# Performance work log

Measured on AMD Instinct MI355X. Metric: run time of the kernel, lower is better.

The kernel has to match this reference:

```python
import jax, jax.numpy as jnp
import numpy as np

B, V, T = 8, 25, 128
C, NH, DK = 256, 8, 32      # hidden_size = NH*DK; dv == dk (required by residual shapes)
DFF, IT = 1024, 4           # FFN hidden (d_in), num_layers
EPS_LN, EPS_BN, SLOPE = 1e-6, 1e-5, 0.01
SCALE = np.float32(1.0 / np.sqrt(DK))


def setup_inputs():
    ks = iter(jax.random.split(jax.random.key(0), 40))
    def w(shape, s=0.05):
        return jax.random.normal(next(ks), shape, jnp.float32) * s
    inp = {'data': jax.random.normal(next(ks), (B, C, V, T), jnp.float32)}
    inp['ln_g'] = jnp.ones((IT, C)); inp['ln_b'] = jnp.zeros((IT, C))
    for p in ('tj', 'tr'):
        for nm in ('q', 'k', 'v'):
            inp[p + '_w' + nm] = w((IT, C, C))
            inp[p + '_b' + nm] = jnp.zeros((IT, C))
        inp[p + '_bn_g'] = jnp.ones((IT, C)); inp[p + '_bn_b'] = jnp.zeros((IT, C))
        inp[p + '_w1'] = w((IT, DFF, C)); inp[p + '_b1'] = jnp.zeros((IT, DFF))
        inp[p + '_w2'] = w((IT, C, DFF)); inp[p + '_b2'] = jnp.zeros((IT, C))
        inp[p + '_fbn_g'] = jnp.ones((IT, C)); inp[p + '_fbn_b'] = jnp.zeros((IT, C))
    return inp


def _bn(x, g, b, axes):
    # train-mode BatchNorm: batch stats, biased variance; channel axis = 1
    m = x.mean(axes, keepdims=True)
    v = ((x - m) ** 2).mean(axes, keepdims=True)
    sh = [1] * x.ndim; sh[1] = -1
    return (x - m) * jax.lax.rsqrt(v + EPS_BN) * g.reshape(sh) + b.reshape(sh)


def _ffn(x, w1, b1, w2, b2, fg, fb):
    # PositionFeedForward on x: [N, C, L] -> [N, C, L]
    xt = jnp.swapaxes(x, 1, 2)                                   # [N, L, C]
    h = jax.nn.relu(jnp.einsum('nlc,fc->nlf', xt, w1) + b1)
    o = jnp.einsum('nlf,cf->nlc', h, w2) + b2 + xt               # residual
    return _bn(jnp.swapaxes(o, 1, 2), fg, fb, (0, 2))


def _tju(x, ax, wq, bq, wk, bk, wv, bv, bn_g, bn_b, w1, b1, w2, b2, fg, fb):
    # sliding-window (3) self-attn + 2 relay tokens; x: [N,C,T], ax: [N,C,2,T]
    N = x.shape[0]
    q = (jnp.einsum('oc,nct->not', wq, x) + bq[:, None]).reshape(N, NH, DK, T)
    k = (jnp.einsum('oc,nct->not', wk, x) + bk[:, None]).reshape(N, NH, DK, T)
    v = (jnp.einsum('oc,nct->not', wv, x) + bv[:, None]).reshape(N, NH, DK, T)
    kp = jnp.pad(k, ((0, 0), (0, 0), (0, 0), (1, 1)))
    vp = jnp.pad(v, ((0, 0), (0, 0), (0, 0), (1, 1)))
    kw = jnp.stack([kp[..., u:u + T] for u in range(3)], axis=3)  # [N,NH,DK,3,T]
    vw = jnp.stack([vp[..., u:u + T] for u in range(3)], axis=3)
    ak = (jnp.einsum('oc,ncat->noat', wk, ax) + bk[:, None, None]).reshape(N, NH, DK, 2, T)
    av = (jnp.einsum('oc,ncat->noat', wv, ax) + bv[:, None, None]).reshape(N, NH, DK, 2, T)
    kk = jnp.concatenate([kw, ak], axis=3)                        # [N,NH,DK,5,T]
    vv = jnp.concatenate([vw, av], axis=3)
    a = jax.nn.softmax(jnp.einsum('nhdt,nhdwt->nhwt', q, kk) * SCALE, axis=2)
    att = jnp.einsum('nhwt,nhdwt->nhdt', a, vv).reshape(N, C, T)
    ret = _bn(x + att, bn_g, bn_b, (0, 2))
    return _ffn(ret, w1, b1, w2, b2, fg, fb)


def _tru(r, y, wq, bq, wk, bk, wv, bv, bn_g, bn_b, w1, b1, w2, b2, fg, fb):
    # relay cross-attention; r: [N,C], y: [N,C,L]
    N, _, L = y.shape
    q = (r @ wq.T + bq).reshape(N, NH, DK)
    k = (jnp.einsum('oc,ncl->nol', wk, y) + bk[:, None]).reshape(N, NH, DK, L)
    v = (jnp.einsum('oc,ncl->nol', wv, y) + bv[:, None]).reshape(N, NH, DK, L)
    a = jax.nn.softmax(jnp.einsum('nhd,nhdl->nhl', q, k) * SCALE, axis=-1)
    att = jnp.einsum('nhl,nhdl->nhd', a, v).reshape(N, C)
    ret = _bn((r + att)[:, :, None], bn_g, bn_b, (0, 2))          # BN over batch
    return _ffn(ret, w1, b1, w2, b2, fg, fb)[:, :, 0]


def _forward(data, ln_g, ln_b, tj, tr):
    N = B * V
    embs = jnp.transpose(data, (0, 2, 1, 3)).reshape(N, C, T)
    nodes, relay = embs, embs.mean(2)                             # relay: [N,C]
    for i in range(IT):
        ax = jnp.concatenate([embs[:, :, None, :],
                              jnp.broadcast_to(relay[:, :, None, None], (N, C, 1, T))], axis=2)
        m = nodes.mean(1, keepdims=True)
        vv = nodes.var(1, keepdims=True)
        xln = (nodes - m) * jax.lax.rsqrt(vv + EPS_LN) * ln_g[i][None, :, None] + ln_b[i][None, :, None]
        nodes = jax.nn.leaky_relu(_tju(xln, ax, *[p[i] for p in tj]), SLOPE)
        y = jnp.concatenate([relay[:, :, None], nodes], axis=2)   # [N,C,T+1]
        relay = jax.nn.leaky_relu(_tru(relay, y, *[p[i] for p in tr]), SLOPE)
    return nodes.reshape(B, V, C, T)


def reference(data, ln_g, ln_b,
              tj_wq, tj_bq, tj_wk, tj_bk, tj_wv, tj_bv, tj_bn_g, tj_bn_b,
              tj_w1, tj_b1, tj_w2, tj_b2, tj_fbn_g, tj_fbn_b,
              tr_wq, tr_bq, tr_wk, tr_bk, tr_wv, tr_bv, tr_bn_g, tr_bn_b,
              tr_w1, tr_b1, tr_w2, tr_b2, tr_fbn_g, tr_fbn_b):
    tj = (tj_wq, tj_bq, tj_wk, tj_bk, tj_wv, tj_bv, tj_bn_g, tj_bn_b,
          tj_w1, tj_b1, tj_w2, tj_b2, tj_fbn_g, tj_fbn_b)
    tr = (tr_wq, tr_bq, tr_wk, tr_bk, tr_wv, tr_bv, tr_bn_g, tr_bn_b,
          tr_w1, tr_b1, tr_w2, tr_b2, tr_fbn_g, tr_fbn_b)
    return _forward(data, ln_g, ln_b, tj, tr)
```

## Files before the change

kernel.cpp:

```cpp
#include <hip/hip_runtime.h>
#include <cstddef>

#define BB   8
#define VV   25
#define TT   128
#define CC   256
#define NHH  8
#define DKK  32
#define DFFF 1024
#define ITER 4
#define NN   (BB*VV)
#define NT   (NN*TT)
#define LL1  (TT+1)
#define EPS_LN 1e-6f
#define EPS_BN 1e-5f
#define SLOPE  0.01f
#define SCALE_F 0.17677669529663687f

typedef unsigned short ushort_t;
typedef __attribute__((ext_vector_type(8))) short short8;
typedef __attribute__((ext_vector_type(4))) short short4_t;
typedef __attribute__((ext_vector_type(4))) float floatx4;

union U8 { short8 v; ushort_t u[8]; };

__device__ __forceinline__ float bf2f(ushort_t u) {
    union { unsigned int i; float f; } x; x.i = ((unsigned int)u) << 16; return x.f;
}
__device__ __forceinline__ ushort_t f2bf(float f) {
    union { float f; unsigned int i; } x; x.f = f;
    unsigned int r = x.i + 0x7FFFu + ((x.i >> 16) & 1u);
    return (ushort_t)(r >> 16);
}
__device__ __forceinline__ float2 bn_fin(float s, float ss) {
    float m = s * (1.0f/NT);
    float var = ss * (1.0f/NT) - m*m; if (var < 0.f) var = 0.f;
    return make_float2(m, rsqrtf(var + EPS_BN));
}

__device__ __forceinline__ void gl_lds16(const ushort_t* g, ushort_t* l) {
    __builtin_amdgcn_global_load_lds(
        (const __attribute__((address_space(1))) unsigned int*)g,
        (__attribute__((address_space(3))) unsigned int*)l,
        16, 0, 0);
}

__device__ __forceinline__ void ld32(const ushort_t* p, float* q) {
    #pragma unroll
    for (int c8 = 0; c8 < 4; c8++) {
        U8 u; u.v = *(const short8*)(p + c8*8);
        #pragma unroll
        for (int j = 0; j < 8; j++) q[c8*8+j] = bf2f(u.u[j]);
    }
}
__device__ __forceinline__ float dot32(const ushort_t* p, const float* q) {
    float s = 0.f;
    #pragma unroll
    for (int c8 = 0; c8 < 4; c8++) {
        U8 u; u.v = *(const short8*)(p + c8*8);
        #pragma unroll
        for (int j = 0; j < 8; j++) s += q[c8*8+j]*bf2f(u.u[j]);
    }
    return s;
}
__device__ __forceinline__ void acc32(const ushort_t* p, float e, float* av) {
    #pragma unroll
    for (int c8 = 0; c8 < 4; c8++) {
        U8 u; u.v = *(const short8*)(p + c8*8);
        #pragma unroll
        for (int j = 0; j < 8; j++) av[c8*8+j] += e*bf2f(u.u[j]);
    }
}

__global__ __launch_bounds__(256) void k_zero(float* __restrict__ p, int n)
{
    int i = blockIdx.x*256 + threadIdx.x;
    if (i < n) p[i] = 0.f;
}
__global__ __launch_bounds__(256) void k_cast2(const float* __restrict__ src,
    ushort_t* __restrict__ dst, int per, int dstride, int total)
{
    int i = blockIdx.x*256 + threadIdx.x;
    if (i < total) dst[(size_t)(i/per)*dstride + (i%per)] = f2bf(src[i]);
}
__global__ __launch_bounds__(256) void k_copy2(const float* __restrict__ src,
    float* __restrict__ dst, int per, int dstride, int total)
{
    int i = blockIdx.x*256 + threadIdx.x;
    if (i < total) dst[(size_t)(i/per)*dstride + (i%per)] = src[i];
}

__global__ __launch_bounds__(128) void k_embed(const float* __restrict__ data,
    float* __restrict__ nodesf, ushort_t* __restrict__ embs_bf, float* __restrict__ relay)
{
    __shared__ float tile[32][TT+1];
    int cc0 = blockIdx.x*32, n = blockIdx.y;
    int b = n / VV, v = n % VV, t = threadIdx.x;
    for (int cl = 0; cl < 32; cl++)
        tile[cl][t] = data[(((size_t)b*CC + cc0 + cl)*VV + v)*TT + t];
    __syncthreads();
    if (t < 32) {
        float s = 0.f;
        for (int tt = 0; tt < TT; tt++) s += tile[t][tt];
        relay[n*CC + cc0 + t] = s * (1.0f/TT);
    }
    #pragma unroll 8
    for (int it = 0; it < 32; it++) {
        int t_l = it*4 + (t >> 5), c_l = t & 31;
        float val = tile[c_l][t_l];
        size_t o = (size_t)(n*TT + t_l)*CC + cc0 + c_l;
        nodesf[o] = val;
        embs_bf[o] = f2bf(val);
    }
}

__global__ __launch_bounds__(256) void k_layernorm(float* __restrict__ x,
    ushort_t* __restrict__ outb, const float* __restrict__ g, const float* __restrict__ b)
{
    int wave = threadIdx.x >> 6, lane = threadIdx.x & 63;
    size_t base = (size_t)(blockIdx.x*4 + wave)*CC + lane*4;
    float4 v = *(float4*)&x[base];
    float s  = v.x + v.y + v.z + v.w;
    float ss = v.x*v.x + v.y*v.y + v.z*v.z + v.w*v.w;
    #pragma unroll
    for (int o = 32; o; o >>= 1) { s += __shfl_xor(s, o); ss += __shfl_xor(ss, o); }
    float m = s * (1.0f/CC);
    float var = ss * (1.0f/CC) - m*m; if (var < 0.f) var = 0.f;
    float rs = rsqrtf(var + EPS_LN);
    float4 gg = *(const float4*)&g[lane*4];
    float4 bb = *(const float4*)&b[lane*4];
    v.x = (v.x - m)*rs*gg.x + bb.x;
    v.y = (v.y - m)*rs*gg.y + bb.y;
    v.z = (v.z - m)*rs*gg.z + bb.z;
    v.w = (v.w - m)*rs*gg.w + bb.w;
    *(float4*)&x[base] = v;
    ushort_t o4[4] = {f2bf(v.x), f2bf(v.y), f2bf(v.z), f2bf(v.w)};
    *(short4_t*)&outb[base] = *(short4_t*)o4;
}

#define FL_RELU  1
#define FL_BF16  2
#define FL_RESBN 4
#define FL_HM    8

#define STAGE(SA, SB, T_) do {                                              \
    gl_lds16(aSrc[0] + (T_)*32, &SA[dstOff[0]]);                            \
    gl_lds16(bSrc[0] + (T_)*32, &SB[dstOff[0]]);                            \
    gl_lds16(aSrc[1] + (T_)*32, &SA[dstOff[1]]);                            \
    gl_lds16(bSrc[1] + (T_)*32, &SB[dstOff[1]]);                            \
    } while (0)

#define COMPUTE(SA, SB) do {                                                \
    short8 af_[4], bf_[4];                                                  \
    _Pragma("unroll")                                                       \
    for (int mi_ = 0; mi_ < 4; mi_++)                                       \
        af_[mi_] = *(const short8*)&SA[aOff[mi_]];                          \
    _Pragma("unroll")                                                       \
    for (int ni_ = 0; ni_ < 4; ni_++)                                       \
        bf_[ni_] = *(const short8*)&SB[bOff[ni_]];                          \
    _Pragma("unroll")                                                       \
    for (int mi_ = 0; mi_ < 4; mi_++)                                       \
        _Pragma("unroll")                                                   \
        for (int ni_ = 0; ni_ < 4; ni_++)                                   \
            acc[mi_][ni_] = __builtin_amdgcn_mfma_f32_16x16x32_bf16(        \
                bf_[ni_], af_[mi_], acc[mi_][ni_], 0, 0, 0);                \
    } while (0)

#define PHASE(CA, CB, PA, PB, T_) do {                                      \
    if ((T_) + 2 < NK) STAGE(PA, PB, (T_) + 2);                             \
    COMPUTE(CA, CB);                                                        \
    if ((T_) + 1 < NK) {                                                    \
        __builtin_amdgcn_sched_barrier(0);                                  \
        if ((T_) + 2 < NK)                                                  \
            asm volatile("s_waitcnt vmcnt(4) lgkmcnt(0)" ::: "memory");     \
        else                                                                \
            asm volatile("s_waitcnt vmcnt(0) lgkmcnt(0)" ::: "memory");     \
        __builtin_amdgcn_s_barrier();                                       \
        __builtin_amdgcn_sched_barrier(0);                                  \
    }                                                                       \
    } while (0)

template<int K, int STATS>
__global__ __launch_bounds__(256) void k_gemm_mfma(
    const ushort_t* A, const ushort_t* B, const float* bias,
    const float* rx, const float* __restrict__ rawms,
    const float* __restrict__ bng, const float* __restrict__ bnb,
    float* outf, ushort_t* outb, int ostride, int ntiles_n, int flags,
    const ushort_t* A2, const ushort_t* B2, const float* bias2,
    ushort_t* outb2, int ostride2, int ntiles_n2,
    float* stats_acc)
{
    __shared__ ushort_t sA0[128*32];
    __shared__ ushort_t sB0[128*32];
    __shared__ ushort_t sA1[128*32];
    __shared__ ushort_t sB1[128*32];
    __shared__ ushort_t sA2[128*32];
    __shared__ ushort_t sB2[128*32];
    const int pid = blockIdx.x;
    const int xcd = pid & 7, idx = pid >> 3;
    const int ntile_tot = ntiles_n + ntiles_n2;
    const int nt_i = idx % ntile_tot;
    const int m0 = (xcd*25 + idx/ntile_tot) * 128;
    const ushort_t* Ap;  const ushort_t* Bp;  const float* biasp;
    ushort_t* outbp;  int ostridep, n0;
    if (nt_i < ntiles_n) {
        Ap = A;  Bp = B;  biasp = bias;  outbp = outb;
        ostridep = ostride;  n0 = nt_i*128;
    } else {
        Ap = A2; Bp = B2; biasp = bias2; outbp = outb2;
        ostridep = ostride2; n0 = (nt_i - ntiles_n)*128;
    }
    const int tid = threadIdx.x;
    const int lane = tid & 63, wave = tid >> 6;
    const int wm = (wave & 1) * 64, wn = (wave >> 1) * 64;
    const int fr = lane >> 4, fc = lane & 15;

    const ushort_t* aSrc[2];
    const ushort_t* bSrc[2];
    int dstOff[2];
    #pragma unroll
    for (int j = 0; j < 2; j++) {
        int s = wave*128 + j*64 + lane;
        int row = s >> 2;
        int kcs = ((s & 3) - (row >> 1)) & 3;
        aSrc[j] = Ap + (size_t)(m0 + row)*K + kcs*8;
        bSrc[j] = Bp + (size_t)(n0 + row)*K + kcs*8;
        dstOff[j] = (wave*128 + j*64)*8;
    }
    int aOff[4], bOff[4];
    #pragma unroll
    for (int mi = 0; mi < 4; mi++) {
        int row = wm + mi*16 + fc;
        aOff[mi] = row*32 + (((fr + (row >> 1)) & 3) * 8);
    }
    #pragma unroll
    for (int ni = 0; ni < 4; ni++) {
        int row = wn + ni*16 + fc;
        bOff[ni] = row*32 + (((fr + (row >> 1)) & 3) * 8);
    }

    floatx4 acc[4][4];
    #pragma unroll
    for (int i = 0; i < 4; i++)
        #pragma unroll
        for (int j = 0; j < 4; j++) acc[i][j] = (floatx4){0.f,0.f,0.f,0.f};

    constexpr int NK = K >> 5;
    STAGE(sA0, sB0, 0);
    if (NK > 1) STAGE(sA1, sB1, 1);
    __builtin_amdgcn_sched_barrier(0);
    if (NK > 1) asm volatile("s_waitcnt vmcnt(4)" ::: "memory");
    else        asm volatile("s_waitcnt vmcnt(0)" ::: "memory");
    __builtin_amdgcn_s_barrier();
    __builtin_amdgcn_sched_barrier(0);

    #pragma unroll
    for (int tb = 0; tb < NK; tb += 3) {
        PHASE(sA0, sB0, sA2, sB2, tb);
        if (tb + 1 < NK) PHASE(sA1, sB1, sA0, sB0, tb + 1);
        if (tb + 2 < NK) PHASE(sA2, sB2, sA1, sB1, tb + 2);
    }

    float st[4][4], sst[4][4];
    if constexpr (STATS) {
        #pragma unroll
        for (int a = 0; a < 4; a++)
            #pragma unroll
            for (int b2_ = 0; b2_ < 4; b2_++) { st[a][b2_] = 0.f; sst[a][b2_] = 0.f; }
    }
    #pragma unroll
    for (int ni = 0; ni < 4; ni++) {
        int nb = n0 + wn + ni*16 + fr*4;
        float4 bias4 = *(const float4*)&biasp[nb];
        float bm[4] = {0,0,0,0}, bs[4] = {0,0,0,0}, bb2[4] = {0,0,0,0};
        if (flags & FL_RESBN) {
            float4 s1 = *(const float4*)&rawms[nb];
            float4 s2 = *(const float4*)&rawms[CC + nb];
            float4 g4 = *(const float4*)&bng[nb];
            float4 b4 = *(const float4*)&bnb[nb];
            float2 f0 = bn_fin(s1.x, s2.x); float2 f1 = bn_fin(s1.y, s2.y);
            float2 f2 = bn_fin(s1.z, s2.z); float2 f3 = bn_fin(s1.w, s2.w);
            bm[0]=f0.x; bm[1]=f1.x; bm[2]=f2.x; bm[3]=f3.x;
            bs[0]=f0.y*g4.x; bs[1]=f1.y*g4.y; bs[2]=f2.y*g4.z; bs[3]=f3.y*g4.w;
            bb2[0]=b4.x; bb2[1]=b4.y; bb2[2]=b4.z; bb2[3]=b4.w;
        }
        float bia[4] = {bias4.x, bias4.y, bias4.z, bias4.w};
        size_t hm_base = ((size_t)(nb >> 5) * NT) * 32 + (nb & 31);
        #pragma unroll
        for (int mi = 0; mi < 4; mi++) {
            int m = m0 + wm + mi*16 + fc;
            size_t idx2 = (flags & FL_HM) ? hm_base + (size_t)m*32
                                          : (size_t)m*ostridep + nb;
            float vals[4];
            #pragma unroll
            for (int r = 0; r < 4; r++) vals[r] = acc[mi][ni][r] + bia[r];
            if (flags & FL_RESBN) {
                float4 rx4 = *(const float4*)&rx[idx2];
                float rxa[4] = {rx4.x, rx4.y, rx4.z, rx4.w};
                #pragma unroll
                for (int r = 0; r < 4; r++)
                    vals[r] += (rxa[r] - bm[r])*bs[r] + bb2[r];
            }
            if (flags & FL_RELU)
                #pragma unroll
                for (int r = 0; r < 4; r++) vals[r] = fmaxf(vals[r], 0.f);
            if constexpr (STATS) {
                #pragma unroll
                for (int r = 0; r < 4; r++) {
                    st[ni][r] += vals[r];
                    sst[ni][r] += vals[r]*vals[r];
                }
            }
            if (flags & FL_BF16) {
                ushort_t o4[4] = {f2bf(vals[0]), f2bf(vals[1]),
                                  f2bf(vals[2]), f2bf(vals[3])};
                *(short4_t*)&outbp[idx2] = *(short4_t*)o4;
            } else {
                float4 ov = make_float4(vals[0], vals[1], vals[2], vals[3]);
                *(float4*)&outf[idx2] = ov;
            }
        }
    }
    if constexpr (STATS) {
        #pragma unroll
        for (int ni = 0; ni < 4; ni++)
            #pragma unroll
            for (int r = 0; r < 4; r++) {
                float s_ = st[ni][r], ss_ = sst[ni][r];
                #pragma unroll
                for (int msk = 1; msk < 16; msk <<= 1) {
                    s_  += __shfl_xor(s_,  msk);
                    ss_ += __shfl_xor(ss_, msk);
                }
                st[ni][r] = s_; sst[ni][r] = ss_;
            }
        if (fc == 0) {
            #pragma unroll
            for (int ni = 0; ni < 4; ni++)
                #pragma unroll
                for (int r = 0; r < 4; r++) {
                    int ch = n0 + wn + ni*16 + fr*4 + r;
                    atomicAdd(&stats_acc[ch],      st[ni][r]);
                    atomicAdd(&stats_acc[CC + ch], sst[ni][r]);
                }
        }
    }
}

__global__ __launch_bounds__(256) void k_sgemm(
    const float* __restrict__ W, const float* __restrict__ X,
    const float* __restrict__ bias, const float* __restrict__ res,
    float* __restrict__ out, int K, int OUT, int do_relu)
{
    __shared__ float sW[16][260];
    __shared__ float sX[16][260];
    int o0 = blockIdx.x*16, n0 = blockIdx.y*16;
    int tx = threadIdx.x, ty = threadIdx.y;
    int tid = ty*16 + tx;
    float acc0 = 0.f, acc1 = 0.f;
    for (int kc = 0; kc < K; kc += 256) {
        #pragma unroll
        for (int j = 0; j < 4; j++) {
            int lin = tid + j*256;
            int row = lin >> 6, c4 = (lin & 63)*4;
            *(float4*)&sW[row][c4] = *(const float4*)&W[(size_t)(o0+row)*K + kc + c4];
            float4 xv = make_float4(0.f,0.f,0.f,0.f);
            if (n0 + row < NN) xv = *(const float4*)&X[(size_t)(n0+row)*K + kc + c4];
            *(float4*)&sX[row][c4] = xv;
        }
        __syncthreads();
        #pragma unroll 8
        for (int k4 = 0; k4 < 64; k4 += 2) {
            float4 w0 = *(const float4*)&sW[tx][k4*4];
            float4 x0 = *(const float4*)&sX[ty][k4*4];
            float4 w1 = *(const float4*)&sW[tx][k4*4+4];
            float4 x1 = *(const float4*)&sX[ty][k4*4+4];
            acc0 += w0.x*x0.x + w0.y*x0.y + w0.z*x0.z + w0.w*x0.w;
            acc1 += w1.x*x1.x + w1.y*x1.y + w1.z*x1.z + w1.w*x1.w;
        }
        __syncthreads();
    }
    float accv = acc0 + acc1;
    int o = o0 + tx, n = n0 + ty;
    if (n < NN) {
        float val = accv + bias[o];
        if (res) val += res[(size_t)n*OUT + o];
        if (do_relu) val = fmaxf(val, 0.f);
        out[(size_t)n*OUT + o] = val;
    }
}

__global__ __launch_bounds__(128) void k_attn_tj(
    const ushort_t* __restrict__ qkv, const ushort_t* __restrict__ ekv,
    const float* __restrict__ rel, const float* __restrict__ xln,
    float* __restrict__ out)
{
    int t = threadIdx.x, h = blockIdx.x, n = blockIdx.y;
    int nt = n*TT + t;
    const ushort_t* qp = qkv + ((size_t)h*NT       + nt)*32;
    const ushort_t* kp = qkv + ((size_t)(8+h)*NT   + nt)*32;
    const ushort_t* vp = qkv + ((size_t)(16+h)*NT  + nt)*32;
    const ushort_t* ep = ekv + ((size_t)h*NT       + nt)*32;
    const ushort_t* evp= ekv + ((size_t)(8+h)*NT   + nt)*32;
    const float*    rp = rel + n*1280 + h*32;

    float qv[32];
    ld32(qp, qv);
    float s0 = 0.f, s1, s2 = 0.f, s3, s4 = 0.f;
    s1 = dot32(kp, qv);
    s3 = dot32(ep, qv);
    #pragma unroll
    for (int j = 0; j < 8; j++) {
        float4 rv4 = *(const float4*)&rp[j*4];
        s4 += qv[j*4]*rv4.x + qv[j*4+1]*rv4.y + qv[j*4+2]*rv4.z + qv[j*4+3]*rv4.w;
    }
    if (t > 0)    s0 = dot32(kp - 32, qv);
    if (t < TT-1) s2 = dot32(kp + 32, qv);

    s0 *= SCALE_F; s1 *= SCALE_F; s2 *= SCALE_F; s3 *= SCALE_F; s4 *= SCALE_F;
    float mx = fmaxf(fmaxf(fmaxf(s0, s1), fmaxf(s2, s3)), s4);
    float e0 = expf(s0-mx), e1 = expf(s1-mx), e2 = expf(s2-mx), e3 = expf(s3-mx), e4 = expf(s4-mx);
    float inv = 1.f/(e0+e1+e2+e3+e4);
    e0 *= inv; e1 *= inv; e2 *= inv; e3 *= inv; e4 *= inv;

    float av[32];
    #pragma unroll
    for (int d = 0; d < 32; d++) av[d] = 0.f;
    acc32(vp, e1, av);
    acc32(evp, e3, av);
    if (t > 0)    acc32(vp - 32, e0, av);
    if (t < TT-1) acc32(vp + 32, e2, av);
    #pragma unroll
    for (int j = 0; j < 8; j++) {
        float4 rv4 = *(const float4*)&rp[256 + j*4];
        av[j*4] += e4*rv4.x; av[j*4+1] += e4*rv4.y; av[j*4+2] += e4*rv4.z; av[j*4+3] += e4*rv4.w;
    }
    const float* xp = xln + (size_t)nt*CC + h*32;
    float* op = out + (size_t)nt*CC + h*32;
    #pragma unroll
    for (int j = 0; j < 8; j++) {
        float4 xv = *(const float4*)&xp[j*4];
        float4 ov;
        ov.x = xv.x + av[j*4]; ov.y = xv.y + av[j*4+1];
        ov.z = xv.z + av[j*4+2]; ov.w = xv.w + av[j*4+3];
        *(float4*)&op[j*4] = ov;
    }
}

__global__ __launch_bounds__(256) void k_bnstats_tm(const float* __restrict__ x,
    float* __restrict__ accum)
{
    __shared__ float lds[8][256];
    int w = threadIdx.x >> 6, lane = threadIdx.x & 63;
    size_t base = (size_t)blockIdx.x*TT*CC;
    float s[4] = {0,0,0,0}, ss[4] = {0,0,0,0};
    for (int tok = w; tok < TT; tok += 4) {
        float4 v = *(const float4*)&x[base + (size_t)tok*CC + lane*4];
        s[0] += v.x; s[1] += v.y; s[2] += v.z; s[3] += v.w;
        ss[0] += v.x*v.x; ss[1] += v.y*v.y; ss[2] += v.z*v.z; ss[3] += v.w*v.w;
    }
    #pragma unroll
    for (int j = 0; j < 4; j++) { lds[w][lane*4+j] = s[j]; lds[4+w][lane*4+j] = ss[j]; }
    __syncthreads();
    int c = threadIdx.x;
    float ps  = lds[0][c]+lds[1][c]+lds[2][c]+lds[3][c];
    float pss = lds[4][c]+lds[5][c]+lds[6][c]+lds[7][c];
    atomicAdd(&accum[c], ps);
    atomicAdd(&accum[CC + c], pss);
}

__global__ __launch_bounds__(256) void k_bn_apply_raw(const float* __restrict__ x,
    const float* __restrict__ acc, const float* __restrict__ g, const float* __restrict__ b,
    ushort_t* __restrict__ outb)
{
    size_t base = ((size_t)blockIdx.x*256 + threadIdx.x)*4;
    int c0 = (int)(base & (CC-1));
    float4 v  = *(const float4*)&x[base];
    float4 a1 = *(const float4*)&acc[c0];
    float4 a2 = *(const float4*)&acc[CC + c0];
    float4 g4 = *(const float4*)&g[c0];
    float4 b4 = *(const float4*)&b[c0];
    float vals[4] = {v.x,v.y,v.z,v.w};
    float s1v[4] = {a1.x,a1.y,a1.z,a1.w};
    float s2v[4] = {a2.x,a2.y,a2.z,a2.w};
    float gg[4] = {g4.x,g4.y,g4.z,g4.w};
    float bb[4] = {b4.x,b4.y,b4.z,b4.w};
    ushort_t o4[4];
    #pragma unroll
    for (int j = 0; j < 4; j++) {
        float2 f = bn_fin(s1v[j], s2v[j]);
        o4[j] = f2bf((vals[j] - f.x)*f.y*gg[j] + bb[j]);
    }
    *(short4_t*)&outb[base] = *(short4_t*)o4;
}

__global__ __launch_bounds__(256) void k_bn_ln(const float* __restrict__ x,
    const float* __restrict__ acc, const float* __restrict__ fg, const float* __restrict__ fb,
    const float* __restrict__ lg, const float* __restrict__ lb,
    float* __restrict__ xlnf, ushort_t* __restrict__ xlnb, ushort_t* __restrict__ nodesb)
{
    int wave = threadIdx.x >> 6, lane = threadIdx.x & 63;
    int c0 = lane*4;
    size_t base = (size_t)(blockIdx.x*4 + wave)*CC + c0;
    float4 v  = *(const float4*)&x[base];
    float4 a1 = *(const float4*)&acc[c0];
    float4 a2 = *(const float4*)&acc[CC + c0];
    float4 g4 = *(const float4*)&fg[c0];
    float4 b4 = *(const float4*)&fb[c0];
    float vals[4] = {v.x,v.y,v.z,v.w};
    float s1v[4] = {a1.x,a1.y,a1.z,a1.w};
    float s2v[4] = {a2.x,a2.y,a2.z,a2.w};
    float gg[4] = {g4.x,g4.y,g4.z,g4.w};
    float bb[4] = {b4.x,b4.y,b4.z,b4.w};
    ushort_t nb4[4];
    #pragma unroll
    for (int j = 0; j < 4; j++) {
        float2 f = bn_fin(s1v[j], s2v[j]);
        float vv = (vals[j] - f.x)*f.y*gg[j] + bb[j];
        vv = vv > 0.f ? vv : SLOPE*vv;
        vals[j] = vv;
        nb4[j] = f2bf(vv);
    }
    *(short4_t*)&nodesb[base] = *(short4_t*)nb4;
    float s  = vals[0]+vals[1]+vals[2]+vals[3];
    float ss = vals[0]*vals[0]+vals[1]*vals[1]+vals[2]*vals[2]+vals[3]*vals[3];
    #pragma unroll
    for (int o = 32; o; o >>= 1) { s += __shfl_xor(s, o); ss += __shfl_xor(ss, o); }
    float m = s * (1.0f/CC);
    float var = ss * (1.0f/CC) - m*m; if (var < 0.f) var = 0.f;
    float rs = rsqrtf(var + EPS_LN);
    float4 lg4 = *(const float4*)&lg[c0];
    float4 lb4 = *(const float4*)&lb[c0];
    float lgv[4] = {lg4.x,lg4.y,lg4.z,lg4.w};
    float lbv[4] = {lb4.x,lb4.y,lb4.z,lb4.w};
    float4 xo;
    ushort_t xb4[4];
    float t0 = (vals[0]-m)*rs*lgv[0] + lbv[0];
    float t1 = (vals[1]-m)*rs*lgv[1] + lbv[1];
    float t2 = (vals[2]-m)*rs*lgv[2] + lbv[2];
    float t3 = (vals[3]-m)*rs*lgv[3] + lbv[3];
    xo.x = t0; xo.y = t1; xo.z = t2; xo.w = t3;
    xb4[0]=f2bf(t0); xb4[1]=f2bf(t1); xb4[2]=f2bf(t2); xb4[3]=f2bf(t3);
    *(float4*)&xlnf[base] = xo;
    *(short4_t*)&xlnb[base] = *(short4_t*)xb4;
}

__global__ __launch_bounds__(256) void k_bn_out_t(const float* __restrict__ x,
    const float* __restrict__ acc, const float* __restrict__ g, const float* __restrict__ b,
    float* __restrict__ out)
{
    __shared__ float tile[64][65];
    int nt0 = blockIdx.x*64, c0 = blockIdx.y*64;
    int w = threadIdx.x >> 6, lane = threadIdx.x & 63;
    int n = nt0 >> 7, t0 = nt0 & 127;
    int c = c0 + lane;
    float2 f = bn_fin(acc[c], acc[CC + c]);
    float gg = f.y*g[c], mm = f.x, bb = b[c];
    #pragma unroll
    for (int it = 0; it < 16; it++) {
        int tok = it*4 + w;
        float v = x[(size_t)(nt0 + tok)*CC + c];
        v = (v - mm)*gg + bb;
        v = v > 0.f ? v : SLOPE*v;
        tile[tok][lane] = v;
    }
    __syncthreads();
    #pragma unroll
    for (int it = 0; it < 16; it++) {
        int c_l = it*4 + w;
        out[(size_t)(n*CC + c0 + c_l)*TT + t0 + lane] = tile[lane][c_l];
    }
}

__global__ __launch_bounds__(64) void k_bn_relay(const float* __restrict__ x,
    float* __restrict__ out, const float* __restrict__ g, const float* __restrict__ b, int leaky)
{
    int c = blockIdx.x, tid = threadIdx.x;
    float s = 0.f, ss = 0.f;
    for (int n = tid; n < NN; n += 64) { float v = x[(size_t)n*CC + c]; s += v; ss += v*v; }
    for (int off = 32; off; off >>= 1) { s += __shfl_down(s, off); ss += __shfl_down(ss, off); }
    float S = __shfl(s, 0), SS = __shfl(ss, 0);
    float m = S / NN;
    float var = SS / NN - m*m; if (var < 0.f) var = 0.f;
    float rs = rsqrtf(var + EPS_BN);
    float gg = g[c]*rs, bb = b[c];
    for (int n = tid; n < NN; n += 64) {
        float v = (x[(size_t)n*CC + c] - m)*gg + bb;
        if (leaky) v = v > 0.f ? v : SLOPE*v;
        out[(size_t)n*CC + c] = v;
    }
}

__global__ __launch_bounds__(64) void k_attn_tr(
    const float* __restrict__ rel, const float* __restrict__ ykv,
    const float* __restrict__ relay, float* __restrict__ out)
{
    int h = blockIdx.x, n = blockIdx.y, tid = threadIdx.x;
    __shared__ float sc[LL1];
    __shared__ float red[64][33];
    float q0[32];
    const float* qp = rel + (size_t)n*1280 + 1024 + h*32;
    #pragma unroll
    for (int j = 0; j < 8; j++) {
        float4 v = *(const float4*)&qp[j*4];
        q0[j*4] = v.x; q0[j*4+1] = v.y; q0[j*4+2] = v.z; q0[j*4+3] = v.w;
    }
    for (int l = tid; l < LL1; l += 64) {
        const float* kp = (l == 0) ? (rel + (size_t)n*1280 + 512 + h*32)
                                   : (ykv + ((size_t)h*NT + n*TT + l-1)*32);
        float s = 0.f;
        #pragma unroll
        for (int j = 0; j < 8; j++) {
            float4 v = *(const float4*)&kp[j*4];
            s += q0[j*4]*v.x + q0[j*4+1]*v.y + q0[j*4+2]*v.z + q0[j*4+3]*v.w;
        }
        sc[l] = s * SCALE_F;
    }
    __syncthreads();
    float mx = -1e30f;
    for (int l = tid; l < LL1; l += 64) mx = fmaxf(mx, sc[l]);
    for (int off = 32; off; off >>= 1) mx = fmaxf(mx, __shfl_xor(mx, off));
    float sum = 0.f;
    for (int l = tid; l < LL1; l += 64) { float e = expf(sc[l]-mx); sc[l] = e; sum += e; }
    for (int off = 32; off; off >>= 1) sum += __shfl_xor(sum, off);
    __syncthreads();
    float av[32];
    #pragma unroll
    for (int d = 0; d < 32; d++) av[d] = 0.f;
    for (int l = tid; l < LL1; l += 64) {
        float e = sc[l];
        const float* vp = (l == 0) ? (rel + (size_t)n*1280 + 768 + h*32)
                                   : (ykv + ((size_t)(8+h)*NT + n*TT + l-1)*32);
        #pragma unroll
        for (int j = 0; j < 8; j++) {
            float4 v = *(const float4*)&vp[j*4];
            av[j*4] += e*v.x; av[j*4+1] += e*v.y; av[j*4+2] += e*v.z; av[j*4+3] += e*v.w;
        }
    }
    #pragma unroll
    for (int d = 0; d < 32; d++) red[tid][d] = av[d];
    __syncthreads();
    if (tid < 32) {
        float a = 0.f;
        for (int k = 0; k < 64; k++) a += red[k][tid];
        a /= sum;
        int idx = n*CC + h*32 + tid;
        out[idx] = relay[idx] + a;
    }
}

extern "C" void kernel_launch(void* const* d_in, const int* in_sizes, int n_in,
                              void* d_out, int out_size, void* d_ws, size_t ws_size,
                              hipStream_t stream)
{
    const float* data    = (const float*)d_in[0];
    const float* ln_g    = (const float*)d_in[1];
    const float* ln_b    = (const float*)d_in[2];
    const float* tj_wq   = (const float*)d_in[3];
    const float* tj_bq   = (const float*)d_in[4];
    const float* tj_wk   = (const float*)d_in[5];
    const float* tj_bk   = (const float*)d_in[6];
    const float* tj_wv   = (const float*)d_in[7];
    const float* tj_bv   = (const float*)d_in[8];
    const float* tj_bn_g = (const float*)d_in[9];
    const float* tj_bn_b = (const float*)d_in[10];
    const float* tj_w1   = (const float*)d_in[11];
    const float* tj_b1   = (const float*)d_in[12];
    const float* tj_w2   = (const float*)d_in[13];
    const float* tj_b2   = (const float*)d_in[14];
    const float* tj_fbn_g= (const float*)d_in[15];
    const float* tj_fbn_b= (const float*)d_in[16];
    const float* tr_wq   = (const float*)d_in[17];
    const float* tr_bq   = (const float*)d_in[18];
    const float* tr_wk   = (const float*)d_in[19];
    const float* tr_bk   = (const float*)d_in[20];
    const float* tr_wv   = (const float*)d_in[21];
    const float* tr_bv   = (const float*)d_in[22];
    const float* tr_bn_g = (const float*)d_in[23];
    const float* tr_bn_b = (const float*)d_in[24];
    const float* tr_w1   = (const float*)d_in[25];
    const float* tr_b1   = (const float*)d_in[26];
    const float* tr_w2   = (const float*)d_in[27];
    const float* tr_b2   = (const float*)d_in[28];
    const float* tr_fbn_g= (const float*)d_in[29];
    const float* tr_fbn_b= (const float*)d_in[30];

    const size_t SZ = (size_t)NT*CC;
    const size_t SZ_NC = (size_t)NN*CC;

    float* ws = (float*)d_ws;
    size_t off = 0;
    auto alloc = [&](size_t nf) { float* p = ws + off; off += nf; return p; };
    float*    nodesf  = alloc(SZ);
    float*    sbuf    = alloc(SZ);
    float*    P1      = alloc(SZ*5/2);
    ushort_t* xs_bf   = (ushort_t*)alloc(SZ/2);
    ushort_t* embs_bf = (ushort_t*)alloc(SZ/2);
    ushort_t* nb_bf   = (ushort_t*)alloc(SZ/2);
    float* accs   = alloc(8*512);
    float* relayA = alloc(SZ_NC);
    float* relayB = alloc(SZ_NC);
    float* rel    = alloc((size_t)NN*1280);
    float* ret0   = alloc(SZ_NC);
    float* rret   = alloc(SZ_NC);
    float* ro     = alloc(SZ_NC);
    float* rh     = alloc((size_t)NN*DFFF);
    ushort_t* wqkv_bf  = (ushort_t*)alloc((size_t)ITER*768*CC/2);
    ushort_t* wkvtr_bf = (ushort_t*)alloc((size_t)ITER*512*CC/2);
    ushort_t* w1_bf    = (ushort_t*)alloc((size_t)ITER*DFFF*CC/2);
    ushort_t* w2_bf    = (ushort_t*)alloc((size_t)ITER*DFFF*CC/2);
    float* wrel  = alloc((size_t)ITER*1280*CC);
    float* brel  = alloc((size_t)ITER*1280);
    float* bqkv  = alloc((size_t)ITER*768);
    float* bkvtr = alloc((size_t)ITER*512);
    (void)ws_size; (void)in_sizes; (void)n_in; (void)out_size;

    ushort_t* qkv_tm = (ushort_t*)P1;
    ushort_t* ekv_tm = qkv_tm + 3*SZ;
    ushort_t* h_us   = (ushort_t*)P1;
    float*    ykv_f  = P1;

    const int TCC = ITER*CC*CC, TFF = ITER*DFFF*CC;
    k_zero<<<16, 256, 0, stream>>>(accs, 8*512);
    k_cast2<<<(TCC+255)/256, 256, 0, stream>>>(tj_wq, wqkv_bf,          65536, 196608, TCC);
    k_cast2<<<(TCC+255)/256, 256, 0, stream>>>(tj_wk, wqkv_bf +  65536, 65536, 196608, TCC);
    k_cast2<<<(TCC+255)/256, 256, 0, stream>>>(tj_wv, wqkv_bf + 131072, 65536, 196608, TCC);
    k_cast2<<<(TCC+255)/256, 256, 0, stream>>>(tr_wk, wkvtr_bf,         65536, 131072, TCC);
    k_cast2<<<(TCC+255)/256, 256, 0, stream>>>(tr_wv, wkvtr_bf + 65536, 65536, 131072, TCC);
    k_cast2<<<(TFF+255)/256, 256, 0, stream>>>(tj_w1, w1_bf, TFF, TFF, TFF);
    k_cast2<<<(TFF+255)/256, 256, 0, stream>>>(tj_w2, w2_bf, TFF, TFF, TFF);
    k_copy2<<<(ITER*256+255)/256, 256, 0, stream>>>(tj_bq, bqkv,       256, 768, ITER*256);
    k_copy2<<<(ITER*256+255)/256, 256, 0, stream>>>(tj_bk, bqkv + 256, 256, 768, ITER*256);
    k_copy2<<<(ITER*256+255)/256, 256, 0, stream>>>(tj_bv, bqkv + 512, 256, 768, ITER*256);
    k_copy2<<<(ITER*256+255)/256, 256, 0, stream>>>(tr_bk, bkvtr,      256, 512, ITER*256);
    k_copy2<<<(ITER*256+255)/256, 256, 0, stream>>>(tr_bv, bkvtr+256,  256, 512, ITER*256);
    k_copy2<<<(TCC+255)/256, 256, 0, stream>>>(tj_wk, wrel,          65536, 327680, TCC);
    k_copy2<<<(TCC+255)/256, 256, 0, stream>>>(tj_wv, wrel +  65536, 65536, 327680, TCC);
    k_copy2<<<(TCC+255)/256, 256, 0, stream>>>(tr_wk, wrel + 131072, 65536, 327680, TCC);
    k_copy2<<<(TCC+255)/256, 256, 0, stream>>>(tr_wv, wrel + 196608, 65536, 327680, TCC);
    k_copy2<<<(TCC+255)/256, 256, 0, stream>>>(tr_wq, wrel + 262144, 65536, 327680, TCC);
    k_copy2<<<(ITER*256+255)/256, 256, 0, stream>>>(tj_bk, brel,        256, 1280, ITER*256);
    k_copy2<<<(ITER*256+255)/256, 256, 0, stream>>>(tj_bv, brel +  256, 256, 1280, ITER*256);
    k_copy2<<<(ITER*256+255)/256, 256, 0, stream>>>(tr_bk, brel +  512, 256, 1280, ITER*256);
    k_copy2<<<(ITER*256+255)/256, 256, 0, stream>>>(tr_bv, brel +  768, 256, 1280, ITER*256);
    k_copy2<<<(ITER*256+255)/256, 256, 0, stream>>>(tr_bq, brel + 1024, 256, 1280, ITER*256);

    k_embed<<<dim3(8, NN), 128, 0, stream>>>(data, nodesf, embs_bf, relayA);
    k_layernorm<<<NT/4, 256, 0, stream>>>(nodesf, xs_bf, ln_g, ln_b);

    float* relay = relayA;
    float* relay_next = relayB;
    dim3 sb16(16, 16);

    for (int i = 0; i < ITER; i++) {
        const size_t woff = (size_t)i*DFFF*CC;
        float* accA = accs + i*1024;
        float* accB = accs + i*1024 + 512;

        k_sgemm<<<dim3((i == ITER-1) ? 32 : 80, 13), sb16, 0, stream>>>(
            wrel + (size_t)i*1280*CC, relay, brel + i*1280, nullptr, rel, CC, 1280, 0);

        k_gemm_mfma<256,0><<<200*10, 256, 0, stream>>>(
            xs_bf, wqkv_bf + (size_t)i*768*CC, bqkv + i*768,
            nullptr, nullptr, nullptr, nullptr,
            nullptr, qkv_tm, 768, 6, FL_BF16 | FL_HM,
            embs_bf, wqkv_bf + (size_t)i*768*CC + 65536, bqkv + i*768 + 256,
            ekv_tm, 512, 4, nullptr);

        k_attn_tj<<<dim3(NHH, NN), 128, 0, stream>>>(qkv_tm, ekv_tm, rel, nodesf, sbuf);

        k_bnstats_tm<<<NN, 256, 0, stream>>>(sbuf, accA);
        k_bn_apply_raw<<<SZ/1024, 256, 0, stream>>>(
            sbuf, accA, tj_bn_g + i*CC, tj_bn_b + i*CC, xs_bf);

        k_gemm_mfma<256,0><<<200*8, 256, 0, stream>>>(
            xs_bf, w1_bf + woff, tj_b1 + i*DFFF, nullptr, nullptr, nullptr, nullptr,
            nullptr, h_us, DFFF, 8, FL_RELU | FL_BF16,
            nullptr, nullptr, nullptr, nullptr, 0, 0, nullptr);
        k_gemm_mfma<1024,1><<<200*2, 256, 0, stream>>>(
            h_us, w2_bf + woff, tj_b2 + i*CC, sbuf, accA, tj_bn_g + i*CC, tj_bn_b + i*CC,
            sbuf, nullptr, CC, 2, FL_RESBN,
            nullptr, nullptr, nullptr, nullptr, 0, 0, accB);

        if (i == ITER-1) {
            k_bn_out_t<<<dim3(NT/64, CC/64), 256, 0, stream>>>(
                sbuf, accB, tj_fbn_g + i*CC, tj_fbn_b + i*CC, (float*)d_out);
            break;
        }
        k_bn_ln<<<NT/4, 256, 0, stream>>>(
            sbuf, accB, tj_fbn_g + i*CC, tj_fbn_b + i*CC,
            ln_g + (i+1)*CC, ln_b + (i+1)*CC, nodesf, xs_bf, nb_bf);

        k_gemm_mfma<256,0><<<200*4, 256, 0, stream>>>(
            nb_bf, wkvtr_bf + (size_t)i*512*CC, bkvtr + i*512,
            nullptr, nullptr, nullptr, nullptr,
            ykv_f, nullptr, 512, 4, FL_HM,
            nullptr, nullptr, nullptr, nullptr, 0, 0, nullptr);

        k_attn_tr<<<dim3(NHH, NN), 64, 0, stream>>>(rel, ykv_f, relay, ret0);
        k_bn_relay<<<CC, 64, 0, stream>>>(ret0, rret, tr_bn_g + i*CC, tr_bn_b + i*CC, 0);

        k_sgemm<<<dim3(DFFF/16, (NN+15)/16), sb16, 0, stream>>>(
            tr_w1 + woff, rret, tr_b1 + i*DFFF, nullptr, rh, CC, DFFF, 1);
        k_sgemm<<<dim3(16, (NN+15)/16), sb16, 0, stream>>>(
            tr_w2 + woff, rh, tr_b2 + i*CC, rret, ro, DFFF, CC, 0);
        k_bn_relay<<<CC, 64, 0, stream>>>(ro, relay_next, tr_fbn_g + i*CC, tr_fbn_b + i*CC, 1);

        float* tmp = relay; relay = relay_next; relay_next = tmp;
    }
}
```

Measured before the change: 1.213 ms.

## Use 8 waves per MFMA GEMM block with specialized A/B staging waves

```diff
diff --git a/kernel.cpp b/kernel.cpp
--- a/kernel.cpp
+++ b/kernel.cpp
@@ -144,44 +144,43 @@
 #define FL_HM    8
 
 #define STAGE(SA, SB, T_) do {                                              \
-    gl_lds16(aSrc[0] + (T_)*32, &SA[dstOff[0]]);                            \
-    gl_lds16(bSrc[0] + (T_)*32, &SB[dstOff[0]]);                            \
-    gl_lds16(aSrc[1] + (T_)*32, &SA[dstOff[1]]);                            \
-    gl_lds16(bSrc[1] + (T_)*32, &SB[dstOff[1]]);                            \
+    ushort_t* db_ = isA ? (SA) : (SB);                                      \
+    gl_lds16(gSrc[0] + (T_)*32, &db_[dstOff[0]]);                           \
+    gl_lds16(gSrc[1] + (T_)*32, &db_[dstOff[1]]);                           \
     } while (0)
 
 #define COMPUTE(SA, SB) do {                                                \
-    short8 af_[4], bf_[4];                                                  \
+    short8 af_[4], bf_[2];                                                  \
     _Pragma("unroll")                                                       \
     for (int mi_ = 0; mi_ < 4; mi_++)                                       \
         af_[mi_] = *(const short8*)&SA[aOff[mi_]];                          \
     _Pragma("unroll")                                                       \
-    for (int ni_ = 0; ni_ < 4; ni_++)                                       \
+    for (int ni_ = 0; ni_ < 2; ni_++)                                       \
         bf_[ni_] = *(const short8*)&SB[bOff[ni_]];                          \
     _Pragma("unroll")                                                       \
     for (int mi_ = 0; mi_ < 4; mi_++)                                       \
         _Pragma("unroll")                                                   \
-        for (int ni_ = 0; ni_ < 4; ni_++)                                   \
+        for (int ni_ = 0; ni_ < 2; ni_++)                                   \
             acc[mi_][ni_] = __builtin_amdgcn_mfma_f32_16x16x32_bf16(        \
                 bf_[ni_], af_[mi_], acc[mi_][ni_], 0, 0, 0);                \
     } while (0)
+
+#define WAITVL(S_) asm volatile("s_waitcnt vmcnt(" S_ ") lgkmcnt(0)" ::: "memory")
 
 #define PHASE(CA, CB, PA, PB, T_) do {                                      \
     if ((T_) + 2 < NK) STAGE(PA, PB, (T_) + 2);                             \
     COMPUTE(CA, CB);                                                        \
     if ((T_) + 1 < NK) {                                                    \
         __builtin_amdgcn_sched_barrier(0);                                  \
-        if ((T_) + 2 < NK)                                                  \
-            asm volatile("s_waitcnt vmcnt(4) lgkmcnt(0)" ::: "memory");     \
-        else                                                                \
-            asm volatile("s_waitcnt vmcnt(0) lgkmcnt(0)" ::: "memory");     \
+        if ((T_) + 2 < NK) WAITVL("2");                                     \
+        else               WAITVL("0");                                     \
         __builtin_amdgcn_s_barrier();                                       \
         __builtin_amdgcn_sched_barrier(0);                                  \
     }                                                                       \
     } while (0)
 
 template<int K, int STATS>
-__global__ __launch_bounds__(256) void k_gemm_mfma(
+__global__ __launch_bounds__(512) void k_gemm_mfma(
     const ushort_t* A, const ushort_t* B, const float* bias,
     const float* rx, const float* __restrict__ rawms,
     const float* __restrict__ bng, const float* __restrict__ bnb,
@@ -212,45 +211,47 @@
     }
     const int tid = threadIdx.x;
     const int lane = tid & 63, wave = tid >> 6;
-    const int wm = (wave & 1) * 64, wn = (wave >> 1) * 64;
+    const int wm = (wave & 1) * 64, wn = (wave >> 1) * 32;
     const int fr = lane >> 4, fc = lane & 15;
 
-    const ushort_t* aSrc[2];
-    const ushort_t* bSrc[2];
+    const bool isA = (wave < 4);
+    const ushort_t* gSrc[2];
     int dstOff[2];
     #pragma unroll
     for (int j = 0; j < 2; j++) {
-        int s = wave*128 + j*64 + lane;
-        int row = s >> 2;
-        int kcs = ((s & 3) - (row >> 1)) & 3;
-        aSrc[j] = Ap + (size_t)(m0 + row)*K + kcs*8;
-        bSrc[j] = Bp + (size_t)(n0 + row)*K + kcs*8;
-        dstOff[j] = (wave*128 + j*64)*8;
-    }
-    int aOff[4], bOff[4];
+        int s  = wave*2 + j;
+        int sl = isA ? s : s - 8;
+        int c  = sl*64 + lane;
+        int row = c >> 2;
+        int kcs = ((c & 3) - (row >> 1)) & 3;
+        gSrc[j] = (isA ? Ap + (size_t)(m0 + row)*K
+                       : Bp + (size_t)(n0 + row)*K) + kcs*8;
+        dstOff[j] = sl*512;
+    }
+    int aOff[4], bOff[2];
     #pragma unroll
     for (int mi = 0; mi < 4; mi++) {
         int row = wm + mi*16 + fc;
         aOff[mi] = row*32 + (((fr + (row >> 1)) & 3) * 8);
     }
     #pragma unroll
-    for (int ni = 0; ni < 4; ni++) {
+    for (int ni = 0; ni < 2; ni++) {
         int row = wn + ni*16 + fc;
         bOff[ni] = row*32 + (((fr + (row >> 1)) & 3) * 8);
     }
 
-    floatx4 acc[4][4];
+    floatx4 acc[4][2];
     #pragma unroll
     for (int i = 0; i < 4; i++)
         #pragma unroll
-        for (int j = 0; j < 4; j++) acc[i][j] = (floatx4){0.f,0.f,0.f,0.f};
+        for (int j = 0; j < 2; j++) acc[i][j] = (floatx4){0.f,0.f,0.f,0.f};
 
     constexpr int NK = K >> 5;
     STAGE(sA0, sB0, 0);
     if (NK > 1) STAGE(sA1, sB1, 1);
     __builtin_amdgcn_sched_barrier(0);
-    if (NK > 1) asm volatile("s_waitcnt vmcnt(4)" ::: "memory");
-    else        asm volatile("s_waitcnt vmcnt(0)" ::: "memory");
+    if (NK > 1) WAITVL("2");
+    else        WAITVL("0");
     __builtin_amdgcn_s_barrier();
     __builtin_amdgcn_sched_barrier(0);
 
@@ -261,15 +262,15 @@
         if (tb + 2 < NK) PHASE(sA2, sB2, sA1, sB1, tb + 2);
     }
 
-    float st[4][4], sst[4][4];
+    float st[2][4], sst[2][4];
     if constexpr (STATS) {
         #pragma unroll
-        for (int a = 0; a < 4; a++)
+        for (int a = 0; a < 2; a++)
             #pragma unroll
             for (int b2_ = 0; b2_ < 4; b2_++) { st[a][b2_] = 0.f; sst[a][b2_] = 0.f; }
     }
     #pragma unroll
-    for (int ni = 0; ni < 4; ni++) {
+    for (int ni = 0; ni < 2; ni++) {
         int nb = n0 + wn + ni*16 + fr*4;
         float4 bias4 = *(const float4*)&biasp[nb];
         float bm[4] = {0,0,0,0}, bs[4] = {0,0,0,0}, bb2[4] = {0,0,0,0};
@@ -323,7 +324,7 @@
     }
     if constexpr (STATS) {
         #pragma unroll
-        for (int ni = 0; ni < 4; ni++)
+        for (int ni = 0; ni < 2; ni++)
             #pragma unroll
             for (int r = 0; r < 4; r++) {
                 float s_ = st[ni][r], ss_ = sst[ni][r];
@@ -336,7 +337,7 @@
             }
         if (fc == 0) {
             #pragma unroll
-            for (int ni = 0; ni < 4; ni++)
+            for (int ni = 0; ni < 2; ni++)
                 #pragma unroll
                 for (int r = 0; r < 4; r++) {
                     int ch = n0 + wn + ni*16 + fr*4 + r;
@@ -760,7 +761,7 @@
         k_sgemm<<<dim3((i == ITER-1) ? 32 : 80, 13), sb16, 0, stream>>>(
             wrel + (size_t)i*1280*CC, relay, brel + i*1280, nullptr, rel, CC, 1280, 0);
 
-        k_gemm_mfma<256,0><<<200*10, 256, 0, stream>>>(
+        k_gemm_mfma<256,0><<<200*10, 512, 0, stream>>>(
             xs_bf, wqkv_bf + (size_t)i*768*CC, bqkv + i*768,
             nullptr, nullptr, nullptr, nullptr,
             nullptr, qkv_tm, 768, 6, FL_BF16 | FL_HM,
@@ -773,11 +774,11 @@
         k_bn_apply_raw<<<SZ/1024, 256, 0, stream>>>(
             sbuf, accA, tj_bn_g + i*CC, tj_bn_b + i*CC, xs_bf);
 
-        k_gemm_mfma<256,0><<<200*8, 256, 0, stream>>>(
+        k_gemm_mfma<256,0><<<200*8, 512, 0, stream>>>(
             xs_bf, w1_bf + woff, tj_b1 + i*DFFF, nullptr, nullptr, nullptr, nullptr,
             nullptr, h_us, DFFF, 8, FL_RELU | FL_BF16,
             nullptr, nullptr, nullptr, nullptr, 0, 0, nullptr);
-        k_gemm_mfma<1024,1><<<200*2, 256, 0, stream>>>(
+        k_gemm_mfma<1024,1><<<200*2, 512, 0, stream>>>(
             h_us, w2_bf + woff, tj_b2 + i*CC, sbuf, accA, tj_bn_g + i*CC, tj_bn_b + i*CC,
             sbuf, nullptr, CC, 2, FL_RESBN,
             nullptr, nullptr, nullptr, nullptr, 0, 0, accB);
@@ -791,7 +792,7 @@
             sbuf, accB, tj_fbn_g + i*CC, tj_fbn_b + i*CC,
             ln_g + (i+1)*CC, ln_b + (i+1)*CC, nodesf, xs_bf, nb_bf);
 
-        k_gemm_mfma<256,0><<<200*4, 256, 0, stream>>>(
+        k_gemm_mfma<256,0><<<200*4, 512, 0, stream>>>(
             nb_bf, wkvtr_bf + (size_t)i*512*CC, bkvtr + i*512,
             nullptr, nullptr, nullptr, nullptr,
             ykv_f, nullptr, 512, 4, FL_HM,
```

Result: faster. 1.155 ms, median of 2 (-4.8%).

## Enlarge MFMA GEMM tile to 256x128 with 512-thread blocks

Applied to the files above, without the earlier changes.

```diff
diff --git a/kernel.cpp b/kernel.cpp
--- a/kernel.cpp
+++ b/kernel.cpp
@@ -143,21 +143,20 @@
 #define FL_RESBN 4
 #define FL_HM    8
 
-#define STAGE(SA, SB, T_) do {                                              \
-    gl_lds16(aSrc[0] + (T_)*32, &SA[dstOff[0]]);                            \
-    gl_lds16(bSrc[0] + (T_)*32, &SB[dstOff[0]]);                            \
-    gl_lds16(aSrc[1] + (T_)*32, &SA[dstOff[1]]);                            \
-    gl_lds16(bSrc[1] + (T_)*32, &SB[dstOff[1]]);                            \
+#define STAGE(SBUF, T_) do {                                                \
+    gl_lds16(gSrc[0] + (T_)*32, &SBUF[dstOff[0]]);                          \
+    gl_lds16(gSrc[1] + (T_)*32, &SBUF[dstOff[1]]);                          \
+    gl_lds16(gSrc[2] + (T_)*32, &SBUF[dstOff[2]]);                          \
     } while (0)
 
-#define COMPUTE(SA, SB) do {                                                \
+#define COMPUTE(SBUF) do {                                                  \
     short8 af_[4], bf_[4];                                                  \
     _Pragma("unroll")                                                       \
     for (int mi_ = 0; mi_ < 4; mi_++)                                       \
-        af_[mi_] = *(const short8*)&SA[aOff[mi_]];                          \
+        af_[mi_] = *(const short8*)&SBUF[aOff[mi_]];                        \
     _Pragma("unroll")                                                       \
     for (int ni_ = 0; ni_ < 4; ni_++)                                       \
-        bf_[ni_] = *(const short8*)&SB[bOff[ni_]];                          \
+        bf_[ni_] = *(const short8*)&SBUF[bOff[ni_]];                        \
     _Pragma("unroll")                                                       \
     for (int mi_ = 0; mi_ < 4; mi_++)                                       \
         _Pragma("unroll")                                                   \
@@ -166,22 +165,22 @@
                 bf_[ni_], af_[mi_], acc[mi_][ni_], 0, 0, 0);                \
     } while (0)
 
-#define PHASE(CA, CB, PA, PB, T_) do {                                      \
-    if ((T_) + 2 < NK) STAGE(PA, PB, (T_) + 2);                             \
-    COMPUTE(CA, CB);                                                        \
+#define WAITVL(S_) asm volatile("s_waitcnt vmcnt(" S_ ") lgkmcnt(0)" ::: "memory")
+
+#define PHASE(CBUF, PBUF, T_) do {                                          \
+    if ((T_) + 2 < NK) STAGE(PBUF, (T_) + 2);                               \
+    COMPUTE(CBUF);                                                          \
     if ((T_) + 1 < NK) {                                                    \
         __builtin_amdgcn_sched_barrier(0);                                  \
-        if ((T_) + 2 < NK)                                                  \
-            asm volatile("s_waitcnt vmcnt(4) lgkmcnt(0)" ::: "memory");     \
-        else                                                                \
-            asm volatile("s_waitcnt vmcnt(0) lgkmcnt(0)" ::: "memory");     \
+        if ((T_) + 2 < NK) WAITVL("3");                                     \
+        else               WAITVL("0");                                     \
         __builtin_amdgcn_s_barrier();                                       \
         __builtin_amdgcn_sched_barrier(0);                                  \
     }                                                                       \
     } while (0)
 
 template<int K, int STATS>
-__global__ __launch_bounds__(256) void k_gemm_mfma(
+__global__ __launch_bounds__(512, STATS ? 2 : 4) void k_gemm_mfma(
     const ushort_t* A, const ushort_t* B, const float* bias,
     const float* rx, const float* __restrict__ rawms,
     const float* __restrict__ bng, const float* __restrict__ bnb,
@@ -190,17 +189,16 @@
     ushort_t* outb2, int ostride2, int ntiles_n2,
     float* stats_acc)
 {
-    __shared__ ushort_t sA0[128*32];
-    __shared__ ushort_t sB0[128*32];
-    __shared__ ushort_t sA1[128*32];
-    __shared__ ushort_t sB1[128*32];
-    __shared__ ushort_t sA2[128*32];
-    __shared__ ushort_t sB2[128*32];
+    __shared__ ushort_t sT0[12288];
+    __shared__ ushort_t sT1[12288];
+    __shared__ ushort_t sT2[12288];
     const int pid = blockIdx.x;
     const int xcd = pid & 7, idx = pid >> 3;
     const int ntile_tot = ntiles_n + ntiles_n2;
     const int nt_i = idx % ntile_tot;
-    const int m0 = (xcd*25 + idx/ntile_tot) * 128;
+    const int mt   = xcd*13 + idx/ntile_tot;
+    if (mt >= 100) return;
+    const int m0 = mt * 256;
     const ushort_t* Ap;  const ushort_t* Bp;  const float* biasp;
     ushort_t* outbp;  int ostridep, n0;
     if (nt_i < ntiles_n) {
@@ -212,20 +210,22 @@
     }
     const int tid = threadIdx.x;
     const int lane = tid & 63, wave = tid >> 6;
-    const int wm = (wave & 1) * 64, wn = (wave >> 1) * 64;
+    const int wm = (wave >> 1) * 64, wn = (wave & 1) * 64;
     const int fr = lane >> 4, fc = lane & 15;
 
-    const ushort_t* aSrc[2];
-    const ushort_t* bSrc[2];
-    int dstOff[2];
-    #pragma unroll
-    for (int j = 0; j < 2; j++) {
-        int s = wave*128 + j*64 + lane;
-        int row = s >> 2;
-        int kcs = ((s & 3) - (row >> 1)) & 3;
-        aSrc[j] = Ap + (size_t)(m0 + row)*K + kcs*8;
-        bSrc[j] = Bp + (size_t)(n0 + row)*K + kcs*8;
-        dstOff[j] = (wave*128 + j*64)*8;
+    const ushort_t* gSrc[3];
+    int dstOff[3];
+    #pragma unroll
+    for (int j = 0; j < 3; j++) {
+        int s  = wave*3 + j;
+        bool isA = (s < 16);
+        int sl = isA ? s : s - 16;
+        int g  = sl*64 + lane;
+        int row = g >> 2;
+        int kcs = ((g & 3) - (row >> 1)) & 3;
+        gSrc[j] = (isA ? Ap + (size_t)(m0 + row)*K
+                       : Bp + (size_t)(n0 + row)*K) + kcs*8;
+        dstOff[j] = (isA ? 0 : 8192) + sl*512;
     }
     int aOff[4], bOff[4];
     #pragma unroll
@@ -236,7 +236,7 @@
     #pragma unroll
     for (int ni = 0; ni < 4; ni++) {
         int row = wn + ni*16 + fc;
-        bOff[ni] = row*32 + (((fr + (row >> 1)) & 3) * 8);
+        bOff[ni] = 8192 + row*32 + (((fr + (row >> 1)) & 3) * 8);
     }
 
     floatx4 acc[4][4];
@@ -246,19 +246,19 @@
         for (int j = 0; j < 4; j++) acc[i][j] = (floatx4){0.f,0.f,0.f,0.f};
 
     constexpr int NK = K >> 5;
-    STAGE(sA0, sB0, 0);
-    if (NK > 1) STAGE(sA1, sB1, 1);
+    STAGE(sT0, 0);
+    if (NK > 1) STAGE(sT1, 1);
     __builtin_amdgcn_sched_barrier(0);
-    if (NK > 1) asm volatile("s_waitcnt vmcnt(4)" ::: "memory");
-    else        asm volatile("s_waitcnt vmcnt(0)" ::: "memory");
+    if (NK > 1) WAITVL("3");
+    else        WAITVL("0");
     __builtin_amdgcn_s_barrier();
     __builtin_amdgcn_sched_barrier(0);
 
     #pragma unroll
     for (int tb = 0; tb < NK; tb += 3) {
-        PHASE(sA0, sB0, sA2, sB2, tb);
-        if (tb + 1 < NK) PHASE(sA1, sB1, sA0, sB0, tb + 1);
-        if (tb + 2 < NK) PHASE(sA2, sB2, sA1, sB1, tb + 2);
+        PHASE(sT0, sT2, tb);
+        if (tb + 1 < NK) PHASE(sT1, sT0, tb + 1);
+        if (tb + 2 < NK) PHASE(sT2, sT1, tb + 2);
     }
 
     float st[4][4], sst[4][4];
@@ -760,7 +760,7 @@
         k_sgemm<<<dim3((i == ITER-1) ? 32 : 80, 13), sb16, 0, stream>>>(
             wrel + (size_t)i*1280*CC, relay, brel + i*1280, nullptr, rel, CC, 1280, 0);
 
-        k_gemm_mfma<256,0><<<200*10, 256, 0, stream>>>(
+        k_gemm_mfma<256,0><<<104*10, 512, 0, stream>>>(
             xs_bf, wqkv_bf + (size_t)i*768*CC, bqkv + i*768,
             nullptr, nullptr, nullptr, nullptr,
             nullptr, qkv_tm, 768, 6, FL_BF16 | FL_HM,
@@ -773,11 +773,11 @@
         k_bn_apply_raw<<<SZ/1024, 256, 0, stream>>>(
             sbuf, accA, tj_bn_g + i*CC, tj_bn_b + i*CC, xs_bf);
 
-        k_gemm_mfma<256,0><<<200*8, 256, 0, stream>>>(
+        k_gemm_mfma<256,0><<<104*8, 512, 0, stream>>>(
             xs_bf, w1_bf + woff, tj_b1 + i*DFFF, nullptr, nullptr, nullptr, nullptr,
             nullptr, h_us, DFFF, 8, FL_RELU | FL_BF16,
             nullptr, nullptr, nullptr, nullptr, 0, 0, nullptr);
-        k_gemm_mfma<1024,1><<<200*2, 256, 0, stream>>>(
+        k_gemm_mfma<1024,1><<<104*2, 512, 0, stream>>>(
             h_us, w2_bf + woff, tj_b2 + i*CC, sbuf, accA, tj_bn_g + i*CC, tj_bn_b + i*CC,
             sbuf, nullptr, CC, 2, FL_RESBN,
             nullptr, nullptr, nullptr, nullptr, 0, 0, accB);
@@ -791,7 +791,7 @@
             sbuf, accB, tj_fbn_g + i*CC, tj_fbn_b + i*CC,
             ln_g + (i+1)*CC, ln_b + (i+1)*CC, nodesf, xs_bf, nb_bf);
 
-        k_gemm_mfma<256,0><<<200*4, 256, 0, stream>>>(
+        k_gemm_mfma<256,0><<<104*4, 512, 0, stream>>>(
             nb_bf, wkvtr_bf + (size_t)i*512*CC, bkvtr + i*512,
             nullptr, nullptr, nullptr, nullptr,
             ykv_f, nullptr, 512, 4, FL_HM,
```

Measured after the change: 1.221 ms. Within noise of the previous version (+0.6%).
